# Performance work log

Hardware: AMD Instinct MI355X
Metric: run time of the kernel (lower is better)

## Reference

```python
import jax, jax.numpy as jnp
import numpy as np

B, N, IN_NF, EDGE_NF = 2, 512, 3, 1
DIM, HEADS, DHEAD, DEPTH = 256, 8, 32, 2
INNER = HEADS * DHEAD
SCALE = DHEAD ** -0.5


def _layernorm(x, g, b):
    m = jnp.mean(x, axis=-1, keepdims=True)
    v = jnp.mean((x - m) ** 2, axis=-1, keepdims=True)
    return (x - m) / jnp.sqrt(v + 1e-5) * g + b


def _rotate_half(x):
    x1, x2 = jnp.split(x, 2, axis=-1)
    return jnp.concatenate([-x2, x1], axis=-1)


def _rotary_freqs(n):
    inv_freq = 1.0 / (10000.0 ** (jnp.arange(0, DHEAD, 2, dtype=jnp.float32) / DHEAD))
    f = jnp.einsum('i,j->ij', jnp.arange(n, dtype=jnp.float32), inv_freq)
    return jnp.concatenate([f, f], axis=-1)  # [n, DHEAD]


def _apply_rotary(freqs, t):
    return t * jnp.cos(freqs) + _rotate_half(t) * jnp.sin(freqs)


def _cdist(x):
    # pairwise L2 distances with grad-safe sqrt at zero (matches torch.cdist fwd)
    d2 = jnp.sum((x[:, :, None, :] - x[:, None, :, :]) ** 2, axis=-1)
    safe = jnp.where(d2 > 0.0, d2, 1.0)
    return jnp.where(d2 > 0.0, jnp.sqrt(safe), 0.0)


def setup_inputs():
    key = jax.random.key(0)
    ks = jax.random.split(key, 12)
    w = lambda k, *shape: jax.random.normal(k, shape, dtype=jnp.float32) * 0.02
    return dict(
        x=jax.random.normal(ks[0], (B, N, IN_NF), dtype=jnp.float32),
        t=jax.random.uniform(ks[1], (B, N, 1), dtype=jnp.float32),
        W_enc=w(ks[2], IN_NF + 1, DIM),
        W_dec=w(ks[3], DIM, IN_NF),
        ln_g=jnp.ones((DEPTH, DIM), jnp.float32),
        ln_b=jnp.zeros((DEPTH, DIM), jnp.float32),
        Wq=w(ks[4], DEPTH, DIM, INNER),
        bq=jnp.zeros((DEPTH, INNER), jnp.float32),
        Wkv=w(ks[5], DEPTH, DIM, 2 * INNER),
        bkv=jnp.zeros((DEPTH, 2 * INNER), jnp.float32),
        We=w(ks[6], DEPTH, EDGE_NF, INNER),
        be=jnp.zeros((DEPTH, INNER), jnp.float32),
        Wo=w(ks[7], DEPTH, INNER, DIM),
        bo=jnp.zeros((DEPTH, DIM), jnp.float32),
        Wg=w(ks[8], DEPTH, 3 * DIM, 1),
    )


def _forward(x, t, W_enc, W_dec, ln_g, ln_b, Wq, bq, Wkv, bkv, We, be, Wo, bo, Wg):
    b, n, _ = x.shape
    edges = _cdist(x)[..., None]                         # [B,N,N,1]
    nodes = jnp.concatenate([x, t], axis=-1) @ W_enc     # [B,N,DIM]
    freqs = _rotary_freqs(n)
    for l in range(DEPTH):
        h = _layernorm(nodes, ln_g[l], ln_b[l])          # PreNorm
        q = (h @ Wq[l] + bq[l]).reshape(b, n, HEADS, DHEAD).transpose(0, 2, 1, 3)
        k, v = jnp.split(h @ Wkv[l] + bkv[l], 2, axis=-1)
        k = k.reshape(b, n, HEADS, DHEAD).transpose(0, 2, 1, 3)
        v = v.reshape(b, n, HEADS, DHEAD).transpose(0, 2, 1, 3)
        e = (edges @ We[l] + be[l]).reshape(b, n, n, HEADS, DHEAD)  # [B,i,j,H,D]
        q = _apply_rotary(freqs, q)
        k = _apply_rotary(freqs, k)
        # sim = q . (k_j + e_ij); split to avoid an extra [B,H,N,N,D] materialization
        sim = (jnp.einsum('bhid,bhjd->bhij', q, k)
               + jnp.einsum('bhid,bijhd->bhij', q, e)) * SCALE
        attn = jax.nn.softmax(sim, axis=-1)
        # out = attn . (v_j + e_ij)
        out = (jnp.einsum('bhij,bhjd->bhid', attn, v)
               + jnp.einsum('bhij,bijhd->bhid', attn, e))
        out = out.transpose(0, 2, 1, 3).reshape(b, n, INNER) @ Wo[l] + bo[l]
        # gated residual
        gate = jax.nn.sigmoid(
            jnp.concatenate([out, nodes, out - nodes], axis=-1) @ Wg[l])
        nodes = out * gate + nodes * (1.0 - gate)
    return nodes @ W_dec                                  # [B,N,IN_NF]


def reference(x, t, W_enc, W_dec, ln_g, ln_b, Wq, bq, Wkv, bkv, We, be, Wo, bo, Wg):
    return _forward(x, t, W_enc, W_dec, ln_g, ln_b, Wq, bq, Wkv, bkv, We, be, Wo, bo, Wg)
```

## Files before the change

kernel.cpp:

```cpp
#include <hip/hip_runtime.h>
#include <math.h>

#define B 2
#define N 512
#define DIM 256
#define HEADS 8
#define DHEAD 32
#define INNER 256
#define DEPTH 2
#define SCALE 0.17677669529663687f

__device__ __forceinline__ float block_sum256(float v, float* red4) {
    #pragma unroll
    for (int o = 32; o; o >>= 1) v += __shfl_xor(v, o);
    int tid = threadIdx.x;
    __syncthreads();
    if ((tid & 63) == 0) red4[tid >> 6] = v;
    __syncthreads();
    return red4[0] + red4[1] + red4[2] + red4[3];
}

__global__ void k_pre(const float* __restrict__ x, const float* __restrict__ t,
                      const float* __restrict__ Wenc,
                      const float* __restrict__ ln_g, const float* __restrict__ ln_b,
                      float* __restrict__ nodes, float* __restrict__ hbuf,
                      float* __restrict__ dist,
                      float* __restrict__ ct, float* __restrict__ st) {
    __shared__ float red4[4];
    __shared__ float xs[N * 3];
    int row = blockIdx.x, d = threadIdx.x;
    int b = row >> 9, i = row & (N - 1);

    if (blockIdx.x < 32) {
        int idx = blockIdx.x * 256 + d;
        int ii = idx >> 4, jj = idx & 15;
        double invf = pow(10000.0, -(double)jj / 16.0);
        double ang = (double)ii * invf;
        ct[idx] = (float)cos(ang);
        st[idx] = (float)sin(ang);
    }

    float x0 = x[row*3+0], x1 = x[row*3+1], x2 = x[row*3+2], tt = t[row];
    float nv = x0*Wenc[d] + x1*Wenc[DIM+d] + x2*Wenc[2*DIM+d] + tt*Wenc[3*DIM+d];
    nodes[row*DIM + d] = nv;
    float mean = block_sum256(nv, red4) * (1.0f/DIM);
    float c = nv - mean;
    float var = block_sum256(c*c, red4) * (1.0f/DIM);
    hbuf[row*DIM + d] = c * (1.0f/sqrtf(var + 1e-5f)) * ln_g[d] + ln_b[d];

    for (int f = d; f < N*3; f += 256) xs[f] = x[b*N*3 + f];
    __syncthreads();
    float xi0 = xs[i*3+0], xi1 = xs[i*3+1], xi2 = xs[i*3+2];
    for (int j = d; j < N; j += 256) {
        float d0 = xi0 - xs[j*3+0], d1 = xi1 - xs[j*3+1], d2 = xi2 - xs[j*3+2];
        float s = d0*d0 + d1*d1 + d2*d2;
        dist[(size_t)row*N + j] = (s > 0.f) ? sqrtf(s) : 0.f;
    }
}

__global__ __launch_bounds__(256, 4)
void k_gemm_qkv(const float* __restrict__ hbuf,
                const float* __restrict__ Wq, const float* __restrict__ bq,
                const float* __restrict__ Wkv, const float* __restrict__ bkv,
                const float* __restrict__ We, const float* __restrict__ be,
                const float* __restrict__ ct, const float* __restrict__ st,
                float* __restrict__ qbuf, float* __restrict__ kbuf, float* __restrict__ vbuf,
                float* __restrict__ qwe, float* __restrict__ qbe, int layer) {
    __shared__ float AT[64][32];
    __shared__ float Bs[64][64];

    int tid = threadIdx.x;
    int mt = blockIdx.x & 31;
    int nt = blockIdx.x >> 5;
    int tx = tid & 15, ty = tid >> 4;
    int n0 = nt * 64;

    const float* Wsrc; int wstride;
    if (n0 < 256) { Wsrc = Wq  + (size_t)layer*256*256 + n0;        wstride = 256; }
    else          { Wsrc = Wkv + (size_t)layer*256*512 + (n0-256);  wstride = 512; }

    float acc[2][4] = {{0,0,0,0},{0,0,0,0}};

    int am = tid & 31, ak = tid >> 5;
    int bn4 = tid & 15, bk = tid >> 4;

    for (int kt = 0; kt < 4; ++kt) {
        int kbase = kt * 64;
        if (kt) __syncthreads();
        {
            const float* src = hbuf + (size_t)(mt*32 + am)*256 + kbase + ak*8;
            float4 a0 = *(const float4*)src;
            float4 a1 = *(const float4*)(src + 4);
            AT[ak*8+0][am]=a0.x; AT[ak*8+1][am]=a0.y; AT[ak*8+2][am]=a0.z; AT[ak*8+3][am]=a0.w;
            AT[ak*8+4][am]=a1.x; AT[ak*8+5][am]=a1.y; AT[ak*8+6][am]=a1.z; AT[ak*8+7][am]=a1.w;
        }
        #pragma unroll
        for (int p = 0; p < 4; ++p) {
            int k = bk + p*16;
            float4 v = *(const float4*)(Wsrc + (size_t)(kbase + k)*wstride + bn4*4);
            *(float4*)&Bs[k][bn4*4] = v;
        }
        __syncthreads();
        #pragma unroll 8
        for (int k = 0; k < 64; ++k) {
            float2 a = *(const float2*)&AT[k][ty*2];
            float4 b = *(const float4*)&Bs[k][tx*4];
            acc[0][0] += a.x*b.x; acc[0][1] += a.x*b.y; acc[0][2] += a.x*b.z; acc[0][3] += a.x*b.w;
            acc[1][0] += a.y*b.x; acc[1][1] += a.y*b.y; acc[1][2] += a.y*b.z; acc[1][3] += a.y*b.w;
        }
    }

    int row = mt*32 + ty*2;
    int n = n0 + tx*4;

    float4 bias4;
    if (n0 < 256) bias4 = *(const float4*)&bq[layer*256 + n];
    else          bias4 = *(const float4*)&bkv[layer*512 + (n - 256)];
    #pragma unroll
    for (int r = 0; r < 2; ++r) {
        acc[r][0] += bias4.x; acc[r][1] += bias4.y; acc[r][2] += bias4.z; acc[r][3] += bias4.w;
    }

    if (n0 >= 512) {
        #pragma unroll
        for (int r = 0; r < 2; ++r) {
            float4 o = make_float4(acc[r][0], acc[r][1], acc[r][2], acc[r][3]);
            *(float4*)&vbuf[(size_t)(row + r)*256 + (n - 512)] = o;
        }
        return;
    }

    float* sh = &Bs[0][0];
    __syncthreads();
    #pragma unroll
    for (int r = 0; r < 2; ++r)
        #pragma unroll
        for (int c = 0; c < 4; ++c)
            sh[(ty*2 + r)*68 + tx*4 + c] = acc[r][c];
    __syncthreads();

    float wep[2] = {0.f, 0.f}, bep[2] = {0.f, 0.f};
    float val[2][4];
    #pragma unroll
    for (int r = 0; r < 2; ++r) {
        int ii = (row + r) & (N-1);
        #pragma unroll
        for (int c = 0; c < 4; ++c) {
            int tc = tx*4 + c;
            int dd = tc & 31, jj = tc & 15;
            float ca = ct[ii*16 + jj], sa = st[ii*16 + jj];
            int ptc = (dd < 16) ? tc + 16 : tc - 16;
            float sgn = (dd < 16) ? -1.f : 1.f;
            float partner = sh[(ty*2 + r)*68 + ptc];
            float rot = acc[r][c]*ca + sgn*partner*sa;
            val[r][c] = rot;
            if (n0 < 256) {
                wep[r] += rot * We[layer*256 + n0 + tc];
                bep[r] += rot * be[layer*256 + n0 + tc];
            }
        }
    }

    float* dst = (n0 < 256) ? qbuf : kbuf;
    int coln = (n0 < 256) ? n : n - 256;
    #pragma unroll
    for (int r = 0; r < 2; ++r) {
        float4 o = make_float4(val[r][0], val[r][1], val[r][2], val[r][3]);
        *(float4*)&dst[(size_t)(row + r)*256 + coln] = o;
    }

    if (n0 < 256) {
        #pragma unroll
        for (int r = 0; r < 2; ++r) {
            wep[r] += __shfl_xor(wep[r], 1); bep[r] += __shfl_xor(bep[r], 1);
            wep[r] += __shfl_xor(wep[r], 2); bep[r] += __shfl_xor(bep[r], 2);
            wep[r] += __shfl_xor(wep[r], 4); bep[r] += __shfl_xor(bep[r], 4);
        }
        if ((tid & 7) == 0) {
            int h = nt*2 + (tx >> 3);
            int bb = row >> 9;
            #pragma unroll
            for (int r = 0; r < 2; ++r) {
                int ii = (row + r) & (N-1);
                qwe[(bb*HEADS + h)*N + ii] = wep[r];
                qbe[(bb*HEADS + h)*N + ii] = bep[r];
            }
        }
    }
}

#define TI 16
__global__ __launch_bounds__(256, 2)
void k_attn(const float* __restrict__ qbuf, const float* __restrict__ kbuf,
            const float* __restrict__ vbuf,
            const float* __restrict__ qwe, const float* __restrict__ qbe,
            const float* __restrict__ dist,
            const float* __restrict__ We, const float* __restrict__ be,
            float* __restrict__ attnout, int layer) {
    __shared__ float Tt[32 * 128];

    int t = threadIdx.x;
    int g = t & 31;
    int r = t >> 5;
    int bid = blockIdx.x;
    int itile = bid & 31;
    int h = (bid >> 5) & (HEADS-1);
    int b = bid >> 8;
    int i0 = itile * TI + r;
    int i1 = i0 + 8;

    int scol = t & 127;
    int d0   = (t >> 7) * 16;

    float q0[32], q1[32];
    {
        const float4* qp0 = (const float4*)(qbuf + (size_t)(b*N + i0) * INNER + h * DHEAD);
        const float4* qp1 = (const float4*)(qbuf + (size_t)(b*N + i1) * INNER + h * DHEAD);
        #pragma unroll
        for (int c = 0; c < 8; ++c) {
            float4 v0 = qp0[c], v1 = qp1[c];
            q0[c*4+0] = v0.x; q0[c*4+1] = v0.y; q0[c*4+2] = v0.z; q0[c*4+3] = v0.w;
            q1[c*4+0] = v1.x; q1[c*4+1] = v1.y; q1[c*4+2] = v1.z; q1[c*4+3] = v1.w;
        }
    }
    float qw0 = qwe[(b*HEADS + h)*N + i0], qb0 = qbe[(b*HEADS + h)*N + i0];
    float qw1 = qwe[(b*HEADS + h)*N + i1], qb1 = qbe[(b*HEADS + h)*N + i1];

    const float* kbase = kbuf + (size_t)b*N*INNER + h*DHEAD;
    const float* vbase = vbuf + (size_t)b*N*INNER + h*DHEAD;
    const float* drow0 = dist + (size_t)(b*N + i0) * N;
    const float* drow1 = dist + (size_t)(b*N + i1) * N;

    float sim0[16], sim1[16];

    #pragma unroll
    for (int jt = 0; jt < 4; ++jt) {
        if (jt) __syncthreads();
        {
            const float* src = kbase + (size_t)(jt*128 + scol) * INNER + d0;
            float4 a0 = *(const float4*)(src + 0);
            float4 a1 = *(const float4*)(src + 4);
            float4 a2 = *(const float4*)(src + 8);
            float4 a3 = *(const float4*)(src + 12);
            Tt[(d0+ 0)*128 + scol] = a0.x; Tt[(d0+ 1)*128 + scol] = a0.y;
            Tt[(d0+ 2)*128 + scol] = a0.z; Tt[(d0+ 3)*128 + scol] = a0.w;
            Tt[(d0+ 4)*128 + scol] = a1.x; Tt[(d0+ 5)*128 + scol] = a1.y;
            Tt[(d0+ 6)*128 + scol] = a1.z; Tt[(d0+ 7)*128 + scol] = a1.w;
            Tt[(d0+ 8)*128 + scol] = a2.x; Tt[(d0+ 9)*128 + scol] = a2.y;
            Tt[(d0+10)*128 + scol] = a2.z; Tt[(d0+11)*128 + scol] = a2.w;
            Tt[(d0+12)*128 + scol] = a3.x; Tt[(d0+13)*128 + scol] = a3.y;
            Tt[(d0+14)*128 + scol] = a3.z; Tt[(d0+15)*128 + scol] = a3.w;
        }
        __syncthreads();
        float4 s0 = make_float4(0.f,0.f,0.f,0.f);
        float4 s1 = make_float4(0.f,0.f,0.f,0.f);
        #pragma unroll
        for (int d = 0; d < 32; ++d) {
            float4 kv = *(const float4*)&Tt[d*128 + g*4];
            float qa = q0[d], qc = q1[d];
            s0.x += qa*kv.x; s0.y += qa*kv.y; s0.z += qa*kv.z; s0.w += qa*kv.w;
            s1.x += qc*kv.x; s1.y += qc*kv.y; s1.z += qc*kv.z; s1.w += qc*kv.w;
        }
        float4 dv0 = *(const float4*)&drow0[jt*128 + g*4];
        float4 dv1 = *(const float4*)&drow1[jt*128 + g*4];
        sim0[jt*4+0] = (s0.x + dv0.x*qw0 + qb0) * SCALE;
        sim0[jt*4+1] = (s0.y + dv0.y*qw0 + qb0) * SCALE;
        sim0[jt*4+2] = (s0.z + dv0.z*qw0 + qb0) * SCALE;
        sim0[jt*4+3] = (s0.w + dv0.w*qw0 + qb0) * SCALE;
        sim1[jt*4+0] = (s1.x + dv1.x*qw1 + qb1) * SCALE;
        sim1[jt*4+1] = (s1.y + dv1.y*qw1 + qb1) * SCALE;
        sim1[jt*4+2] = (s1.z + dv1.z*qw1 + qb1) * SCALE;
        sim1[jt*4+3] = (s1.w + dv1.w*qw1 + qb1) * SCALE;
    }

    float mx0 = -1e30f, mx1 = -1e30f;
    #pragma unroll
    for (int v = 0; v < 16; ++v) { mx0 = fmaxf(mx0, sim0[v]); mx1 = fmaxf(mx1, sim1[v]); }
    #pragma unroll
    for (int o = 1; o <= 16; o <<= 1) {
        mx0 = fmaxf(mx0, __shfl_xor(mx0, o));
        mx1 = fmaxf(mx1, __shfl_xor(mx1, o));
    }

    float ls0 = 0.f, ld0 = 0.f, ls1 = 0.f, ld1 = 0.f;
    #pragma unroll
    for (int jt = 0; jt < 4; ++jt) {
        float4 dv0 = *(const float4*)&drow0[jt*128 + g*4];
        float4 dv1 = *(const float4*)&drow1[jt*128 + g*4];
        float a0[4] = {dv0.x,dv0.y,dv0.z,dv0.w};
        float a1[4] = {dv1.x,dv1.y,dv1.z,dv1.w};
        #pragma unroll
        for (int u = 0; u < 4; ++u) {
            float p0 = __expf(sim0[jt*4+u] - mx0);
            float p1 = __expf(sim1[jt*4+u] - mx1);
            sim0[jt*4+u] = p0; sim1[jt*4+u] = p1;
            ls0 += p0; ld0 += p0 * a0[u];
            ls1 += p1; ld1 += p1 * a1[u];
        }
    }
    #pragma unroll
    for (int o = 1; o <= 16; o <<= 1) {
        ls0 += __shfl_xor(ls0, o); ld0 += __shfl_xor(ld0, o);
        ls1 += __shfl_xor(ls1, o); ld1 += __shfl_xor(ld1, o);
    }

    float acc0[32], acc1[32];
    #pragma unroll
    for (int d = 0; d < 32; ++d) { acc0[d] = 0.f; acc1[d] = 0.f; }

    #pragma unroll
    for (int jt = 0; jt < 4; ++jt) {
        __syncthreads();
        {
            const float* src = vbase + (size_t)(jt*128 + scol) * INNER + d0;
            float4 a0 = *(const float4*)(src + 0);
            float4 a1 = *(const float4*)(src + 4);
            float4 a2 = *(const float4*)(src + 8);
            float4 a3 = *(const float4*)(src + 12);
            Tt[(d0+ 0)*128 + scol] = a0.x; Tt[(d0+ 1)*128 + scol] = a0.y;
            Tt[(d0+ 2)*128 + scol] = a0.z; Tt[(d0+ 3)*128 + scol] = a0.w;
            Tt[(d0+ 4)*128 + scol] = a1.x; Tt[(d0+ 5)*128 + scol] = a1.y;
            Tt[(d0+ 6)*128 + scol] = a1.z; Tt[(d0+ 7)*128 + scol] = a1.w;
            Tt[(d0+ 8)*128 + scol] = a2.x; Tt[(d0+ 9)*128 + scol] = a2.y;
            Tt[(d0+10)*128 + scol] = a2.z; Tt[(d0+11)*128 + scol] = a2.w;
            Tt[(d0+12)*128 + scol] = a3.x; Tt[(d0+13)*128 + scol] = a3.y;
            Tt[(d0+14)*128 + scol] = a3.z; Tt[(d0+15)*128 + scol] = a3.w;
        }
        __syncthreads();
        float p00 = sim0[jt*4+0], p01 = sim0[jt*4+1], p02 = sim0[jt*4+2], p03 = sim0[jt*4+3];
        float p10 = sim1[jt*4+0], p11 = sim1[jt*4+1], p12 = sim1[jt*4+2], p13 = sim1[jt*4+3];
        #pragma unroll
        for (int d = 0; d < 32; ++d) {
            float4 vv = *(const float4*)&Tt[d*128 + g*4];
            acc0[d] += p00*vv.x + p01*vv.y + p02*vv.z + p03*vv.w;
            acc1[d] += p10*vv.x + p11*vv.y + p12*vv.z + p13*vv.w;
        }
    }

    #pragma unroll
    for (int d = 0; d < 32; ++d) {
        #pragma unroll
        for (int o = 1; o <= 16; o <<= 1) {
            acc0[d] += __shfl_xor(acc0[d], o);
            acc1[d] += __shfl_xor(acc1[d], o);
        }
    }

    float il0 = 1.0f / ls0, il1 = 1.0f / ls1;
    float ad0 = ld0 * il0, ad1 = ld1 * il1;
    float o0 = acc0[0], o1 = acc1[0];
    #pragma unroll
    for (int d = 1; d < 32; ++d) if (g == d) { o0 = acc0[d]; o1 = acc1[d]; }
    float wv = We[layer*INNER + h*DHEAD + g];
    float bv = be[layer*INNER + h*DHEAD + g];
    attnout[(size_t)(b*N + i0)*INNER + h*DHEAD + g] = o0*il0 + ad0*wv + bv;
    attnout[(size_t)(b*N + i1)*INNER + h*DHEAD + g] = o1*il1 + ad1*wv + bv;
}

__global__ __launch_bounds__(256, 4)
void k_gemm_o(const float* __restrict__ attnout, const float* __restrict__ Wo,
              const float* __restrict__ bo, float* __restrict__ obuf, int layer) {
    __shared__ float AT[64][32];
    __shared__ float Bs[64][32];
    int tid = threadIdx.x;
    int mt = blockIdx.x & 31, nt = blockIdx.x >> 5;
    int tx = tid & 7, ty = tid >> 3;

    float acc[4] = {0,0,0,0};
    int am = tid & 31, ak = tid >> 5;
    int bn4 = tid & 7, bk = tid >> 3;
    const float* Wsrc = Wo + (size_t)layer*256*256 + nt*32;

    for (int kt = 0; kt < 4; ++kt) {
        int kbase = kt * 64;
        if (kt) __syncthreads();
        {
            const float* src = attnout + (size_t)(mt*32 + am)*256 + kbase + ak*8;
            float4 a0 = *(const float4*)src;
            float4 a1 = *(const float4*)(src + 4);
            AT[ak*8+0][am]=a0.x; AT[ak*8+1][am]=a0.y; AT[ak*8+2][am]=a0.z; AT[ak*8+3][am]=a0.w;
            AT[ak*8+4][am]=a1.x; AT[ak*8+5][am]=a1.y; AT[ak*8+6][am]=a1.z; AT[ak*8+7][am]=a1.w;
        }
        #pragma unroll
        for (int p = 0; p < 2; ++p) {
            int k = bk + p*32;
            *(float4*)&Bs[k][bn4*4] = *(const float4*)(Wsrc + (size_t)(kbase + k)*256 + bn4*4);
        }
        __syncthreads();
        #pragma unroll 8
        for (int k = 0; k < 64; ++k) {
            float a = AT[k][ty];
            float4 b = *(const float4*)&Bs[k][tx*4];
            acc[0] += a*b.x; acc[1] += a*b.y; acc[2] += a*b.z; acc[3] += a*b.w;
        }
    }
    int row = mt*32 + ty, n = nt*32 + tx*4;
    float4 bias = *(const float4*)&bo[layer*256 + n];
    float4 o = make_float4(acc[0]+bias.x, acc[1]+bias.y, acc[2]+bias.z, acc[3]+bias.w);
    *(float4*)&obuf[(size_t)row*256 + n] = o;
}

__global__ void k_gate_ln(const float* __restrict__ obuf, const float* __restrict__ Wg,
                          const float* __restrict__ ln_g, const float* __restrict__ ln_b,
                          const float* __restrict__ Wdec,
                          float* __restrict__ nodes, float* __restrict__ hbuf,
                          float* __restrict__ out, int layer) {
    __shared__ float red4[4];
    int row = blockIdx.x, d = threadIdx.x;
    float o  = obuf[row*DIM + d];
    float nd = nodes[row*DIM + d];
    const float* Wgl = Wg + layer*3*DIM;
    float s = o*Wgl[d] + nd*Wgl[DIM+d] + (o-nd)*Wgl[2*DIM+d];
    float tot = block_sum256(s, red4);
    float gate = 1.0f/(1.0f + __expf(-tot));
    float nn = o*gate + nd*(1.0f - gate);
    nodes[row*DIM + d] = nn;
    if (layer == 0) {
        float mean = block_sum256(nn, red4) * (1.0f/DIM);
        float c = nn - mean;
        float var = block_sum256(c*c, red4) * (1.0f/DIM);
        hbuf[row*DIM + d] = c * (1.0f/sqrtf(var + 1e-5f)) * ln_g[DIM + d] + ln_b[DIM + d];
    } else {
        float s0 = block_sum256(nn * Wdec[d*3+0], red4);
        float s1 = block_sum256(nn * Wdec[d*3+1], red4);
        float s2 = block_sum256(nn * Wdec[d*3+2], red4);
        if (d == 0) { out[row*3+0] = s0; out[row*3+1] = s1; out[row*3+2] = s2; }
    }
}

extern "C" void kernel_launch(void* const* d_in, const int* in_sizes, int n_in,
                              void* d_out, int out_size, void* d_ws, size_t ws_size,
                              hipStream_t stream) {
    const float* x     = (const float*)d_in[0];
    const float* t     = (const float*)d_in[1];
    const float* W_enc = (const float*)d_in[2];
    const float* W_dec = (const float*)d_in[3];
    const float* ln_g  = (const float*)d_in[4];
    const float* ln_b  = (const float*)d_in[5];
    const float* Wq    = (const float*)d_in[6];
    const float* bq    = (const float*)d_in[7];
    const float* Wkv   = (const float*)d_in[8];
    const float* bkv   = (const float*)d_in[9];
    const float* We    = (const float*)d_in[10];
    const float* be    = (const float*)d_in[11];
    const float* Wo    = (const float*)d_in[12];
    const float* bo    = (const float*)d_in[13];
    const float* Wg    = (const float*)d_in[14];
    float* out = (float*)d_out;

    float* ws = (float*)d_ws;
    float* nodes   = ws;
    float* dist    = nodes   + B*N*DIM;
    float* hbuf    = dist    + B*N*N;
    float* qbuf    = hbuf    + B*N*DIM;
    float* kbuf    = qbuf    + B*N*INNER;
    float* vbuf    = kbuf    + B*N*INNER;
    float* qwe     = vbuf    + B*N*INNER;
    float* qbe     = qwe     + B*HEADS*N;
    float* attnout = qbe     + B*HEADS*N;
    float* obuf    = attnout + B*N*INNER;
    float* ct      = obuf    + B*N*DIM;
    float* st      = ct      + N*16;

    k_pre<<<B*N, DIM, 0, stream>>>(x, t, W_enc, ln_g, ln_b, nodes, hbuf, dist, ct, st);
    for (int l = 0; l < DEPTH; ++l) {
        k_gemm_qkv<<<384, 256, 0, stream>>>(hbuf, Wq, bq, Wkv, bkv, We, be, ct, st,
                                            qbuf, kbuf, vbuf, qwe, qbe, l);
        k_attn<<<B*HEADS*(N/TI), 256, 0, stream>>>(qbuf, kbuf, vbuf, qwe, qbe, dist, We, be,
                                                   attnout, l);
        k_gemm_o<<<256, 256, 0, stream>>>(attnout, Wo, bo, obuf, l);
        k_gate_ln<<<B*N, DIM, 0, stream>>>(obuf, Wg, ln_g, ln_b, W_dec, nodes, hbuf, out, l);
    }
}
```

Before: 112.9 us.

## Fuse output projection with gated residual and layernorm into one kernel

Replaces the tiled Wo GEMM kernel and the separate gate/layernorm kernel with one kernel in which each wavefront computes a full 256-wide output row, then applies the gate, residual, layernorm or decoder projection using wave-level shuffles. This removes one launch per layer and the obuf round trip through global memory, and swaps block reductions for wave shuffles. In exchange, each block of 4 rows streams the whole 256x256 Wo matrix from global or L2 memory with no shared-memory reuse, so weight traffic per row rises considerably and only 256 blocks run.

```diff
diff --git a/kernel.cpp b/kernel.cpp
--- a/kernel.cpp
+++ b/kernel.cpp
@@ -358,73 +358,76 @@
 }
 
 __global__ __launch_bounds__(256, 4)
-void k_gemm_o(const float* __restrict__ attnout, const float* __restrict__ Wo,
-              const float* __restrict__ bo, float* __restrict__ obuf, int layer) {
-    __shared__ float AT[64][32];
-    __shared__ float Bs[64][32];
+void k_ogate(const float* __restrict__ attnout,
+             const float* __restrict__ Wo, const float* __restrict__ bo,
+             const float* __restrict__ Wg,
+             const float* __restrict__ ln_g, const float* __restrict__ ln_b,
+             const float* __restrict__ Wdec,
+             float* __restrict__ nodes, float* __restrict__ hbuf,
+             float* __restrict__ out, int layer) {
+    __shared__ float arow[4*256];
     int tid = threadIdx.x;
-    int mt = blockIdx.x & 31, nt = blockIdx.x >> 5;
-    int tx = tid & 7, ty = tid >> 3;
-
-    float acc[4] = {0,0,0,0};
-    int am = tid & 31, ak = tid >> 5;
-    int bn4 = tid & 7, bk = tid >> 3;
-    const float* Wsrc = Wo + (size_t)layer*256*256 + nt*32;
-
-    for (int kt = 0; kt < 4; ++kt) {
-        int kbase = kt * 64;
-        if (kt) __syncthreads();
-        {
-            const float* src = attnout + (size_t)(mt*32 + am)*256 + kbase + ak*8;
-            float4 a0 = *(const float4*)src;
-            float4 a1 = *(const float4*)(src + 4);
-            AT[ak*8+0][am]=a0.x; AT[ak*8+1][am]=a0.y; AT[ak*8+2][am]=a0.z; AT[ak*8+3][am]=a0.w;
-            AT[ak*8+4][am]=a1.x; AT[ak*8+5][am]=a1.y; AT[ak*8+6][am]=a1.z; AT[ak*8+7][am]=a1.w;
-        }
-        #pragma unroll
-        for (int p = 0; p < 2; ++p) {
-            int k = bk + p*32;
-            *(float4*)&Bs[k][bn4*4] = *(const float4*)(Wsrc + (size_t)(kbase + k)*256 + bn4*4);
-        }
-        __syncthreads();
-        #pragma unroll 8
-        for (int k = 0; k < 64; ++k) {
-            float a = AT[k][ty];
-            float4 b = *(const float4*)&Bs[k][tx*4];
-            acc[0] += a*b.x; acc[1] += a*b.y; acc[2] += a*b.z; acc[3] += a*b.w;
-        }
-    }
-    int row = mt*32 + ty, n = nt*32 + tx*4;
-    float4 bias = *(const float4*)&bo[layer*256 + n];
-    float4 o = make_float4(acc[0]+bias.x, acc[1]+bias.y, acc[2]+bias.z, acc[3]+bias.w);
-    *(float4*)&obuf[(size_t)row*256 + n] = o;
-}
-
-__global__ void k_gate_ln(const float* __restrict__ obuf, const float* __restrict__ Wg,
-                          const float* __restrict__ ln_g, const float* __restrict__ ln_b,
-                          const float* __restrict__ Wdec,
-                          float* __restrict__ nodes, float* __restrict__ hbuf,
-                          float* __restrict__ out, int layer) {
-    __shared__ float red4[4];
-    int row = blockIdx.x, d = threadIdx.x;
-    float o  = obuf[row*DIM + d];
-    float nd = nodes[row*DIM + d];
+    int w = tid >> 6;
+    int lane = tid & 63;
+    int rg = blockIdx.x*4 + w;
+    int c0 = lane*4;
+
+    *(float4*)&arow[tid*4] = *(const float4*)&attnout[(size_t)blockIdx.x*1024 + tid*4];
+    __syncthreads();
+
+    const float* Wol = Wo + (size_t)layer*256*256;
+    float4 bias = *(const float4*)&bo[layer*256 + c0];
+    float a0 = bias.x, a1 = bias.y, a2 = bias.z, a3 = bias.w;
+    const float* ar = &arow[w*256];
+    #pragma unroll 8
+    for (int k = 0; k < 256; ++k) {
+        float a = ar[k];
+        float4 wv = *(const float4*)&Wol[(size_t)k*256 + c0];
+        a0 += a*wv.x; a1 += a*wv.y; a2 += a*wv.z; a3 += a*wv.w;
+    }
+
+    float4 nd = *(const float4*)&nodes[(size_t)rg*256 + c0];
     const float* Wgl = Wg + layer*3*DIM;
-    float s = o*Wgl[d] + nd*Wgl[DIM+d] + (o-nd)*Wgl[2*DIM+d];
-    float tot = block_sum256(s, red4);
-    float gate = 1.0f/(1.0f + __expf(-tot));
-    float nn = o*gate + nd*(1.0f - gate);
-    nodes[row*DIM + d] = nn;
+    float4 g1 = *(const float4*)&Wgl[c0];
+    float4 g2 = *(const float4*)&Wgl[DIM + c0];
+    float4 g3 = *(const float4*)&Wgl[2*DIM + c0];
+    float sp = a0*g1.x + nd.x*g2.x + (a0-nd.x)*g3.x
+             + a1*g1.y + nd.y*g2.y + (a1-nd.y)*g3.y
+             + a2*g1.z + nd.z*g2.z + (a2-nd.z)*g3.z
+             + a3*g1.w + nd.w*g2.w + (a3-nd.w)*g3.w;
+    #pragma unroll
+    for (int o = 32; o; o >>= 1) sp += __shfl_xor(sp, o);
+    float gate = 1.0f/(1.0f + __expf(-sp));
+    float n0 = a0*gate + nd.x*(1.0f-gate);
+    float n1 = a1*gate + nd.y*(1.0f-gate);
+    float n2 = a2*gate + nd.z*(1.0f-gate);
+    float n3 = a3*gate + nd.w*(1.0f-gate);
+    *(float4*)&nodes[(size_t)rg*256 + c0] = make_float4(n0, n1, n2, n3);
+
     if (layer == 0) {
-        float mean = block_sum256(nn, red4) * (1.0f/DIM);
-        float c = nn - mean;
-        float var = block_sum256(c*c, red4) * (1.0f/DIM);
-        hbuf[row*DIM + d] = c * (1.0f/sqrtf(var + 1e-5f)) * ln_g[DIM + d] + ln_b[DIM + d];
+        float ms = n0 + n1 + n2 + n3;
+        #pragma unroll
+        for (int o = 32; o; o >>= 1) ms += __shfl_xor(ms, o);
+        float mean = ms * (1.0f/DIM);
+        float c0v = n0-mean, c1v = n1-mean, c2v = n2-mean, c3v = n3-mean;
+        float vs = c0v*c0v + c1v*c1v + c2v*c2v + c3v*c3v;
+        #pragma unroll
+        for (int o = 32; o; o >>= 1) vs += __shfl_xor(vs, o);
+        float rs = 1.0f/sqrtf(vs*(1.0f/DIM) + 1e-5f);
+        float4 lg = *(const float4*)&ln_g[DIM + c0];
+        float4 lb = *(const float4*)&ln_b[DIM + c0];
+        float4 h = make_float4(c0v*rs*lg.x + lb.x, c1v*rs*lg.y + lb.y,
+                               c2v*rs*lg.z + lb.z, c3v*rs*lg.w + lb.w);
+        *(float4*)&hbuf[(size_t)rg*256 + c0] = h;
     } else {
-        float s0 = block_sum256(nn * Wdec[d*3+0], red4);
-        float s1 = block_sum256(nn * Wdec[d*3+1], red4);
-        float s2 = block_sum256(nn * Wdec[d*3+2], red4);
-        if (d == 0) { out[row*3+0] = s0; out[row*3+1] = s1; out[row*3+2] = s2; }
+        float s0 = n0*Wdec[(c0+0)*3+0] + n1*Wdec[(c0+1)*3+0] + n2*Wdec[(c0+2)*3+0] + n3*Wdec[(c0+3)*3+0];
+        float s1 = n0*Wdec[(c0+0)*3+1] + n1*Wdec[(c0+1)*3+1] + n2*Wdec[(c0+2)*3+1] + n3*Wdec[(c0+3)*3+1];
+        float s2 = n0*Wdec[(c0+0)*3+2] + n1*Wdec[(c0+1)*3+2] + n2*Wdec[(c0+2)*3+2] + n3*Wdec[(c0+3)*3+2];
+        #pragma unroll
+        for (int o = 32; o; o >>= 1) {
+            s0 += __shfl_xor(s0, o); s1 += __shfl_xor(s1, o); s2 += __shfl_xor(s2, o);
+        }
+        if (lane == 0) { out[rg*3+0] = s0; out[rg*3+1] = s1; out[rg*3+2] = s2; }
     }
 }
 
@@ -458,8 +461,7 @@
     float* qwe     = vbuf    + B*N*INNER;
     float* qbe     = qwe     + B*HEADS*N;
     float* attnout = qbe     + B*HEADS*N;
-    float* obuf    = attnout + B*N*INNER;
-    float* ct      = obuf    + B*N*DIM;
+    float* ct      = attnout + B*N*INNER;
     float* st      = ct      + N*16;
 
     k_pre<<<B*N, DIM, 0, stream>>>(x, t, W_enc, ln_g, ln_b, nodes, hbuf, dist, ct, st);
@@ -468,7 +470,7 @@
                                             qbuf, kbuf, vbuf, qwe, qbe, l);
         k_attn<<<B*HEADS*(N/TI), 256, 0, stream>>>(qbuf, kbuf, vbuf, qwe, qbe, dist, We, be,
                                                    attnout, l);
-        k_gemm_o<<<256, 256, 0, stream>>>(attnout, Wo, bo, obuf, l);
-        k_gate_ln<<<B*N, DIM, 0, stream>>>(obuf, Wg, ln_g, ln_b, W_dec, nodes, hbuf, out, l);
-    }
-}
+        k_ogate<<<B*N/4, 256, 0, stream>>>(attnout, Wo, bo, Wg, ln_g, ln_b, W_dec,
+                                           nodes, hbuf, out, l);
+    }
+}
```

Result: slower. 116.1 us (+2.9%).
